# Optimization experiments

Measured on AMD Instinct MI355X. Metric: run time of the kernel, lower is better.

## Reference

```python
import jax, jax.numpy as jnp
import numpy as np

N, L, D, H = 4, 2048, 512, 8
DK = D // H


def setup_inputs() -> dict:
    key = jax.random.key(0)
    ks = jax.random.split(key, 12)
    s = 1.0 / np.sqrt(D)
    x_q = jax.random.normal(ks[0], (N, L, D), dtype=jnp.float32)
    x_k = jax.random.normal(ks[1], (N, L, D), dtype=jnp.float32)
    x_v = jax.random.normal(ks[2], (N, L, D), dtype=jnp.float32)
    # causal attention mask (1 = keep)
    attention_mask = jnp.tril(jnp.ones((L, L), dtype=jnp.int32))
    # padding mask: random valid lengths in [L//2, L], 1 = keep
    lengths = jax.random.randint(ks[3], (N,), L // 2, L + 1)
    padding_mask = (jnp.arange(L)[None, :] < lengths[:, None]).astype(jnp.int32)
    Wq = jax.random.uniform(ks[4], (D, D), jnp.float32, -s, s)
    bq = jax.random.uniform(ks[5], (D,), jnp.float32, -s, s)
    Wk = jax.random.uniform(ks[6], (D, D), jnp.float32, -s, s)
    bk = jax.random.uniform(ks[7], (D,), jnp.float32, -s, s)
    Wv = jax.random.uniform(ks[8], (D, D), jnp.float32, -s, s)
    bv = jax.random.uniform(ks[9], (D,), jnp.float32, -s, s)
    Wo = jax.random.uniform(ks[10], (D, D), jnp.float32, -s, s)
    bo = jax.random.uniform(ks[11], (D,), jnp.float32, -s, s)
    return {"x_q": x_q, "x_k": x_k, "x_v": x_v,
            "padding_mask": padding_mask, "attention_mask": attention_mask,
            "Wq": Wq, "bq": bq, "Wk": Wk, "bk": bk,
            "Wv": Wv, "bv": bv, "Wo": Wo, "bo": bo}


def reference(x_q, x_k, x_v, padding_mask, attention_mask,
              Wq, bq, Wk, bk, Wv, bv, Wo, bo):
    n, lq, _ = x_q.shape
    lkv = x_k.shape[1]
    Q = (x_q @ Wq.T + bq).reshape(n, lq, H, DK)
    K = (x_k @ Wk.T + bk).reshape(n, lkv, H, DK)
    V = (x_v @ Wv.T + bv).reshape(n, lkv, H, DK)
    # score: [n, lq, lkv, H]
    score = jnp.einsum('nihd,njhd->nijh', Q, K) / np.sqrt(DK)
    score = jnp.where(attention_mask.reshape(1, lq, lkv, 1) == 0, -jnp.inf, score)
    score = jnp.where(padding_mask.reshape(n, 1, lkv, 1) == 0, -jnp.inf, score)
    score = jax.nn.softmax(score, axis=2)
    value = jnp.einsum('nijh,njhd->nihd', score, V).reshape(n, lq, D)
    return value @ Wo.T + bo
```

## Files before the change

kernel.cpp:

```cpp
#include <hip/hip_runtime.h>
#include <hip/hip_bf16.h>

#define NB 4
#define LSEQ 2048
#define DMODEL 512
#define NH 8
#define DKH 64

typedef __attribute__((ext_vector_type(8))) short bf16x8;
typedef __attribute__((ext_vector_type(4))) float f32x4;

__device__ __forceinline__ unsigned short f2bf(float f) {
  __hip_bfloat16 h = __float2bfloat16(f);
  return __builtin_bit_cast(unsigned short, h);
}
__device__ __forceinline__ float bf2f(unsigned short u) {
  unsigned int x = ((unsigned int)u) << 16;
  return __builtin_bit_cast(float, x);
}

#define GLD16(gsrc, ldst)                                                     \
  __builtin_amdgcn_global_load_lds(                                           \
      (const __attribute__((address_space(1))) unsigned int*)(gsrc),          \
      (__attribute__((address_space(3))) unsigned int*)(ldst), 16, 0, 0)

__global__ __launch_bounds__(256) void prep(
    const float* __restrict__ s0, const float* __restrict__ s1,
    const float* __restrict__ s2, unsigned short* __restrict__ hi,
    unsigned short* __restrict__ lo,
    const float* __restrict__ w0, const float* __restrict__ w1,
    const float* __restrict__ w2, const float* __restrict__ w3,
    unsigned short* __restrict__ whi, unsigned short* __restrict__ wlo,
    int nz) {
  const int bid = blockIdx.x;
  const int actBlocks = nz << 12;
  const float* src;
  unsigned short *dh, *dl;
  int i;
  if (bid < actBlocks) {
    const int z = bid >> 12;
    src = (z == 0) ? s0 : (z == 1) ? s1 : s2;
    const size_t off = (size_t)z * ((size_t)NB * LSEQ * DMODEL);
    i = ((bid & 4095) * 256 + threadIdx.x) * 4;
    dh = hi + off; dl = lo + off;
  } else {
    const int wb = bid - actBlocks;
    const int wi = wb >> 8;
    src = (wi == 0) ? w0 : (wi == 1) ? w1 : (wi == 2) ? w2 : w3;
    const size_t off = (size_t)wi * 262144;
    i = ((wb & 255) * 256 + threadIdx.x) * 4;
    dh = whi + off; dl = wlo + off;
  }
  const float4 v = *(const float4*)&src[i];
  ushort4 h, l;
  h.x = f2bf(v.x); l.x = f2bf(v.x - bf2f(h.x));
  h.y = f2bf(v.y); l.y = f2bf(v.y - bf2f(h.y));
  h.z = f2bf(v.z); l.z = f2bf(v.z - bf2f(h.z));
  h.w = f2bf(v.w); l.w = f2bf(v.w - bf2f(h.w));
  *(ushort4*)&dh[i] = h;
  *(ushort4*)&dl[i] = l;
}

template <int BF16OUT>
__global__ __launch_bounds__(256, 1) void gemm3(
    const unsigned short* __restrict__ AhB, const unsigned short* __restrict__ AlB,
    const unsigned short* __restrict__ WhB, const unsigned short* __restrict__ WlB,
    const float* __restrict__ bias0, const float* __restrict__ bias1,
    const float* __restrict__ bias2, void* __restrict__ CB,
    unsigned short* __restrict__ VtOut, int zbase, int scaleq) {
  __shared__ unsigned short AsH[2][128 * 64];
  __shared__ unsigned short AsL[2][128 * 64];
  __shared__ unsigned short WsH[2][128 * 64];
  __shared__ unsigned short WsL[2][128 * 64];
  const size_t matE = (size_t)NB * LSEQ * DMODEL;

  const int bid = blockIdx.x;
  const int off = bid >> 3;
  const int P = (bid & 7) + 8 * (off >> 2);
  const int bx = off & 3;
  const int by = P & 63;
  const int z = P >> 6;
  const int zz = z + zbase;

  const unsigned short* Ah = AhB + (size_t)z * matE;
  const unsigned short* Al = AlB + (size_t)z * matE;
  const unsigned short* Wh = WhB + (size_t)z * DMODEL * DMODEL;
  const unsigned short* Wl = WlB + (size_t)z * DMODEL * DMODEL;
  const float* bias = (zz == 0) ? bias0 : (zz == 1) ? bias1 : bias2;
  const float scale = (scaleq && zz == 0) ? 0.18033688011112042f : 1.0f;
  const bool vt = BF16OUT && (zz == 2);

  const int tid = threadIdx.x;
  const int w = tid >> 6, lane = tid & 63;
  const int l15 = lane & 15, l4 = lane >> 4;
  const int bn = bx * 128;
  const int bm = by * 128;
  const int wm = (w >> 1) * 64, wn = (w & 1) * 64;
  const int lr8 = lane >> 3, slot = lane & 7;

  float bi[4];
#pragma unroll
  for (int nf = 0; nf < 4; ++nf) bi[nf] = bias[bn + wn + nf * 16 + l15];

  f32x4 acc[4][4] = {};

#define STAGE_G(buf, k0)                                                      \
  {                                                                           \
    _Pragma("unroll")                                                         \
    for (int j = 0; j < 4; ++j) {                                             \
      const int seg = w * 32 + j * 8;                                         \
      const int row = seg + lr8;                                              \
      const int sc = slot ^ (row & 7);                                        \
      const size_t gA = (size_t)(bm + row) * DMODEL + (k0) + sc * 8;          \
      const size_t gW = (size_t)(bn + row) * DMODEL + (k0) + sc * 8;          \
      GLD16(Ah + gA, &AsH[buf][seg * 64]);                                    \
      GLD16(Al + gA, &AsL[buf][seg * 64]);                                    \
      GLD16(Wh + gW, &WsH[buf][seg * 64]);                                    \
      GLD16(Wl + gW, &WsL[buf][seg * 64]);                                    \
    }                                                                         \
  }

  STAGE_G(0, 0);

#pragma unroll 1
  for (int it = 0; it < 8; ++it) {
    const int cur = it & 1;
    if (it < 7) {
      STAGE_G(cur ^ 1, (it + 1) * 64);
      asm volatile("s_waitcnt vmcnt(16)" ::: "memory");
    } else {
      asm volatile("s_waitcnt vmcnt(0)" ::: "memory");
    }
    __builtin_amdgcn_s_barrier();

#pragma unroll
    for (int ks = 0; ks < 2; ++ks) {
      bf16x8 afh[4], afl[4], wfh[4], wfl[4];
#pragma unroll
      for (int mf = 0; mf < 4; ++mf) {
        const int row = wm + mf * 16 + l15;
        const int sl = (ks * 4 + l4) ^ (row & 7);
        afh[mf] = *(const bf16x8*)&AsH[cur][row * 64 + sl * 8];
        afl[mf] = *(const bf16x8*)&AsL[cur][row * 64 + sl * 8];
      }
#pragma unroll
      for (int nf = 0; nf < 4; ++nf) {
        const int row = wn + nf * 16 + l15;
        const int sl = (ks * 4 + l4) ^ (row & 7);
        wfh[nf] = *(const bf16x8*)&WsH[cur][row * 64 + sl * 8];
        wfl[nf] = *(const bf16x8*)&WsL[cur][row * 64 + sl * 8];
      }
#pragma unroll
      for (int mf = 0; mf < 4; ++mf)
#pragma unroll
        for (int nf = 0; nf < 4; ++nf) {
          acc[mf][nf] = __builtin_amdgcn_mfma_f32_16x16x32_bf16(afh[mf], wfh[nf], acc[mf][nf], 0, 0, 0);
          acc[mf][nf] = __builtin_amdgcn_mfma_f32_16x16x32_bf16(afh[mf], wfl[nf], acc[mf][nf], 0, 0, 0);
          acc[mf][nf] = __builtin_amdgcn_mfma_f32_16x16x32_bf16(afl[mf], wfh[nf], acc[mf][nf], 0, 0, 0);
        }
    }
    __builtin_amdgcn_s_barrier();
  }
#undef STAGE_G

#pragma unroll
  for (int mf = 0; mf < 4; ++mf)
#pragma unroll
    for (int r = 0; r < 4; ++r) {
      const size_t row = (size_t)(bm + wm + mf * 16 + l4 * 4 + r);
#pragma unroll
      for (int nf = 0; nf < 4; ++nf) {
        const float v = (acc[mf][nf][r] + bi[nf]) * scale;
        const int col = bn + wn + nf * 16 + l15;
        if (vt) {
          const int tok = (int)row & (LSEQ - 1);
          const int nn = (int)row >> 11;
          const int hh = col >> 6, dd = col & 63;
          VtOut[((((size_t)nn * NH + hh) * DKH + dd) << 11) + tok] = f2bf(v);
        } else {
          const size_t o = row * DMODEL + col;
          if (BF16OUT) ((unsigned short*)CB)[z * matE + o] = f2bf(v);
          else         ((float*)CB)[z * matE + o] = v;
        }
      }
    }
}

__global__ __launch_bounds__(256, 3) void flash_mfma(
    const unsigned short* __restrict__ Qb, const unsigned short* __restrict__ Kb,
    const unsigned short* __restrict__ Vt, const int* __restrict__ pad,
    unsigned short* __restrict__ OH, unsigned short* __restrict__ OL) {
  __shared__ unsigned short Ks[2][64 * 64];
  __shared__ unsigned short Vs[2][64 * 64];
  __shared__ unsigned short Ps[64 * 64];
  __shared__ int s_nt;

  const int tid = threadIdx.x;
  const int bid = blockIdx.x;
  const int sub = bid >> 3;
  const int nh = (bid & 7) * 4 + (sub & 3);
  const int qt = 31 - (sub >> 2);
  const int n = nh >> 3, h = nh & 7;
  const int w = tid >> 6, lane = tid & 63;
  const int l15 = lane & 15, l4 = lane >> 4;
  const int lr8 = lane >> 3, slot = lane & 7;

  {
    const int v = (tid < 32) ? pad[(size_t)n * LSEQ + tid * 64] : 1;
    if (tid < 64) {
      const unsigned long long b = __ballot(v == 0);
      if (tid == 0) s_nt = b ? (int)(__ffsll(b) - 1) : 32;
    }
  }
  __syncthreads();
  const int nt = s_nt;

  int plast[4];
#pragma unroll
  for (int f = 0; f < 4; ++f)
    plast[f] = pad[(size_t)n * LSEQ + (nt - 1) * 64 + f * 16 + l15];

  bf16x8 vones;
  {
    const short o = (l15 == 0) ? (short)0x3F80 : (short)0;
#pragma unroll
    for (int j = 0; j < 8; ++j) vones[j] = o;
  }

  const size_t qrow = (size_t)(n * LSEQ + qt * 64 + w * 16 + l15) * DMODEL + h * DKH;
  const bf16x8 qa0 = *(const bf16x8*)(Qb + qrow + l4 * 8);
  const bf16x8 qa1 = *(const bf16x8*)(Qb + qrow + 32 + l4 * 8);

  f32x4 Oacc[5] = {};
  float m_[4];
#pragma unroll
  for (int r = 0; r < 4; ++r) m_[r] = -1e30f;

  const int ktend = (qt + 1 < nt) ? (qt + 1) : nt;

#pragma unroll
  for (int j = 0; j < 2; ++j) {
    const int seg = w * 16 + j * 8;
    const int row = seg + lr8;
    const int sc = slot ^ (row & 7);
    GLD16(Kb + (size_t)(n * LSEQ + row) * DMODEL + h * DKH + sc * 8, &Ks[0][seg * 64]);
    GLD16(Vt + ((size_t)nh * DKH + row) * LSEQ + sc * 8, &Vs[0][seg * 64]);
  }
  asm volatile("s_waitcnt vmcnt(0)" ::: "memory");
  __builtin_amdgcn_s_barrier();

#pragma unroll 1
  for (int kt = 0; kt < ktend; ++kt) {
    const int cur = kt & 1;
    if (kt + 1 < ktend) {
      const int nb = cur ^ 1;
#pragma unroll
      for (int j = 0; j < 2; ++j) {
        const int seg = w * 16 + j * 8;
        const int row = seg + lr8;
        const int sc = slot ^ (row & 7);
        GLD16(Kb + (size_t)(n * LSEQ + (kt + 1) * 64 + row) * DMODEL + h * DKH + sc * 8,
              &Ks[nb][seg * 64]);
        GLD16(Vt + ((size_t)nh * DKH + row) * LSEQ + (kt + 1) * 64 + sc * 8,
              &Vs[nb][seg * 64]);
      }
    }

    f32x4 S[4] = {};
#pragma unroll
    for (int f = 0; f < 4; ++f) {
      const int kr = f * 16 + l15;
      const int swz = kr & 7;
      const bf16x8 b0 = *(const bf16x8*)&Ks[cur][kr * 64 + ((l4 ^ swz) * 8)];
      S[f] = __builtin_amdgcn_mfma_f32_16x16x32_bf16(qa0, b0, S[f], 0, 0, 0);
      const bf16x8 b1 = *(const bf16x8*)&Ks[cur][kr * 64 + (((4 + l4) ^ swz) * 8)];
      S[f] = __builtin_amdgcn_mfma_f32_16x16x32_bf16(qa1, b1, S[f], 0, 0, 0);
    }

    if (kt == nt - 1) {
#pragma unroll
      for (int f = 0; f < 4; ++f)
        if (!plast[f]) {
#pragma unroll
          for (int r = 0; r < 4; ++r) S[f][r] = -1e30f;
        }
    }
    if (kt == qt) {
#pragma unroll
      for (int f = 0; f < 4; ++f) {
        const int col = f * 16 + l15;
#pragma unroll
        for (int r = 0; r < 4; ++r)
          if (col > w * 16 + l4 * 4 + r) S[f][r] = -1e30f;
      }
    }

    float pmax[4];
#pragma unroll
    for (int r = 0; r < 4; ++r)
      pmax[r] = fmaxf(fmaxf(S[0][r], S[1][r]), fmaxf(S[2][r], S[3][r]));
    const bool cond = (pmax[0] <= m_[0] + 11.f) && (pmax[1] <= m_[1] + 11.f) &&
                      (pmax[2] <= m_[2] + 11.f) && (pmax[3] <= m_[3] + 11.f);
    if (!__all(cond)) {
#pragma unroll
      for (int r = 0; r < 4; ++r) {
        float mx = pmax[r];
        mx = fmaxf(mx, __shfl_xor(mx, 1, 64));
        mx = fmaxf(mx, __shfl_xor(mx, 2, 64));
        mx = fmaxf(mx, __shfl_xor(mx, 4, 64));
        mx = fmaxf(mx, __shfl_xor(mx, 8, 64));
        const float mnew = fmaxf(m_[r], mx);
        const float alpha = exp2f(m_[r] - mnew);
        m_[r] = mnew;
#pragma unroll
        for (int f = 0; f < 5; ++f) Oacc[f][r] *= alpha;
      }
    }

#pragma unroll
    for (int r = 0; r < 4; ++r) {
      const int prow = w * 16 + l4 * 4 + r;
      const int psw = prow & 7;
#pragma unroll
      for (int f = 0; f < 4; ++f) {
        const float p = exp2f(S[f][r] - m_[r]);
        const int c16 = 2 * f + (l15 >> 3);
        Ps[prow * 64 + ((c16 ^ psw) * 8) + (lane & 7)] = f2bf(p);
      }
    }

#pragma unroll
    for (int ks = 0; ks < 2; ++ks) {
      const int prow = w * 16 + l15;
      const bf16x8 pa = *(const bf16x8*)&Ps[prow * 64 + (((ks * 4 + l4) ^ (prow & 7)) * 8)];
      Oacc[4] = __builtin_amdgcn_mfma_f32_16x16x32_bf16(pa, vones, Oacc[4], 0, 0, 0);
#pragma unroll
      for (int f = 0; f < 4; ++f) {
        const int vr = f * 16 + l15;
        const bf16x8 vb = *(const bf16x8*)&Vs[cur][vr * 64 + (((ks * 4 + l4) ^ (vr & 7)) * 8)];
        Oacc[f] = __builtin_amdgcn_mfma_f32_16x16x32_bf16(pa, vb, Oacc[f], 0, 0, 0);
      }
    }

    asm volatile("s_waitcnt vmcnt(0)" ::: "memory");
    __builtin_amdgcn_s_barrier();
  }

#pragma unroll
  for (int r = 0; r < 4; ++r) {
    const float lr = __shfl(Oacc[4][r], l4 << 4, 64);
    const float inv = 1.0f / lr;
    const size_t orow = (size_t)(n * LSEQ + qt * 64 + w * 16 + l4 * 4 + r) * DMODEL + h * DKH;
#pragma unroll
    for (int f = 0; f < 4; ++f) {
      const float v = Oacc[f][r] * inv;
      const unsigned short hh = f2bf(v);
      OH[orow + f * 16 + l15] = hh;
      OL[orow + f * 16 + l15] = f2bf(v - bf2f(hh));
    }
  }
}

extern "C" void kernel_launch(void* const* d_in, const int* in_sizes, int n_in,
                              void* d_out, int out_size, void* d_ws, size_t ws_size,
                              hipStream_t stream) {
  const float* x_q = (const float*)d_in[0];
  const float* x_k = (const float*)d_in[1];
  const float* x_v = (const float*)d_in[2];
  const int*   pad = (const int*)d_in[3];
  const float* Wq = (const float*)d_in[5];  const float* bq = (const float*)d_in[6];
  const float* Wk = (const float*)d_in[7];  const float* bk = (const float*)d_in[8];
  const float* Wv = (const float*)d_in[9];  const float* bv = (const float*)d_in[10];
  const float* Wo = (const float*)d_in[11]; const float* bo = (const float*)d_in[12];
  float* out = (float*)d_out;

  const size_t matE = (size_t)NB * LSEQ * DMODEL;
  const size_t wE = (size_t)DMODEL * DMODEL;
  unsigned short* base = (unsigned short*)d_ws;
  const size_t needB = (size_t)(9 * matE + 8 * wE) * 2;
  const bool batched = ws_size >= needB;

  if (batched) {
    unsigned short* Ah3 = base;
    unsigned short* Al3 = base + 3 * matE;
    unsigned short* QKV = base + 6 * matE;
    unsigned short* WhA = base + 9 * matE;
    unsigned short* WlA = WhA + 4 * wE;
    unsigned short* Vt  = QKV + 2 * matE;
    unsigned short* OHp = base;
    unsigned short* OLp = base + matE;

    prep<<<13312, 256, 0, stream>>>(x_q, x_k, x_v, Ah3, Al3,
                                    Wq, Wk, Wv, Wo, WhA, WlA, 3);
    gemm3<1><<<768, 256, 0, stream>>>(Ah3, Al3, WhA, WlA, bq, bk, bv,
                                      (void*)QKV, Vt, 0, 1);
    flash_mfma<<<1024, 256, 0, stream>>>(QKV, QKV + matE, Vt, pad, OHp, OLp);
    gemm3<0><<<256, 256, 0, stream>>>(OHp, OLp, WhA + 3 * wE, WlA + 3 * wE,
                                      bo, bo, bo, (void*)out, nullptr, 0, 0);
  } else {
    unsigned short* Ah = base;
    unsigned short* Al = base + matE;
    unsigned short* QKV = base + 2 * matE;
    unsigned short* WhA = base + 5 * matE;
    unsigned short* WlA = WhA + 4 * wE;
    unsigned short* Vt  = QKV + 2 * matE;
    unsigned short* OHp = base;
    unsigned short* OLp = base + matE;

    const float* xs[3] = {x_q, x_k, x_v};
    const float* bs[3] = {bq, bk, bv};
    for (int z = 0; z < 3; ++z) {
      prep<<<(z == 0) ? 5120 : 4096, 256, 0, stream>>>(
          xs[z], xs[z], xs[z], Ah, Al, Wq, Wk, Wv, Wo, WhA, WlA, 1);
      gemm3<1><<<256, 256, 0, stream>>>(Ah, Al, WhA + z * wE, WlA + z * wE,
                                        bs[z], bs[z], bs[z],
                                        (void*)(QKV + z * matE), Vt, z, 1);
    }
    flash_mfma<<<1024, 256, 0, stream>>>(QKV, QKV + matE, Vt, pad, OHp, OLp);
    gemm3<0><<<256, 256, 0, stream>>>(OHp, OLp, WhA + 3 * wE, WlA + 3 * wE,
                                      bo, bo, bo, (void*)out, nullptr, 0, 0);
  }
}
```

Before: 241.5 us.

## Replace bf16 hi/lo split GEMMs with single-pass fp16 across pipeline

Drops the three-MFMA bf16 hi/lo split emulation of fp32 in the projection GEMMs and writes one fp16 copy of activations and weights instead. Attention and all MFMAs switch from bf16 to fp16. This cuts MFMA work in the GEMMs to a third, halves the staging traffic and LDS use (which allows two blocks per CU), and removes the low-part writes from prep and flash. The cost is accuracy: inputs and the attention output lose precision, and fp16's narrower range could matter for unscaled values.

```diff
diff --git a/kernel.cpp b/kernel.cpp
--- a/kernel.cpp
+++ b/kernel.cpp
@@ -1,5 +1,4 @@
 #include <hip/hip_runtime.h>
-#include <hip/hip_bf16.h>
 
 #define NB 4
 #define LSEQ 2048
@@ -7,16 +6,12 @@
 #define NH 8
 #define DKH 64
 
-typedef __attribute__((ext_vector_type(8))) short bf16x8;
+typedef __attribute__((ext_vector_type(8))) _Float16 f16x8;
 typedef __attribute__((ext_vector_type(4))) float f32x4;
 
-__device__ __forceinline__ unsigned short f2bf(float f) {
-  __hip_bfloat16 h = __float2bfloat16(f);
+__device__ __forceinline__ unsigned short f2h(float f) {
+  _Float16 h = (_Float16)f;
   return __builtin_bit_cast(unsigned short, h);
-}
-__device__ __forceinline__ float bf2f(unsigned short u) {
-  unsigned int x = ((unsigned int)u) << 16;
-  return __builtin_bit_cast(float, x);
 }
 
 #define GLD16(gsrc, ldst)                                                     \
@@ -26,52 +21,41 @@
 
 __global__ __launch_bounds__(256) void prep(
     const float* __restrict__ s0, const float* __restrict__ s1,
-    const float* __restrict__ s2, unsigned short* __restrict__ hi,
-    unsigned short* __restrict__ lo,
+    const float* __restrict__ s2, unsigned short* __restrict__ xh,
     const float* __restrict__ w0, const float* __restrict__ w1,
     const float* __restrict__ w2, const float* __restrict__ w3,
-    unsigned short* __restrict__ whi, unsigned short* __restrict__ wlo,
-    int nz) {
+    unsigned short* __restrict__ wh, int nz) {
   const int bid = blockIdx.x;
   const int actBlocks = nz << 12;
   const float* src;
-  unsigned short *dh, *dl;
+  unsigned short* dst;
   int i;
   if (bid < actBlocks) {
     const int z = bid >> 12;
     src = (z == 0) ? s0 : (z == 1) ? s1 : s2;
-    const size_t off = (size_t)z * ((size_t)NB * LSEQ * DMODEL);
+    dst = xh + (size_t)z * ((size_t)NB * LSEQ * DMODEL);
     i = ((bid & 4095) * 256 + threadIdx.x) * 4;
-    dh = hi + off; dl = lo + off;
   } else {
     const int wb = bid - actBlocks;
     const int wi = wb >> 8;
     src = (wi == 0) ? w0 : (wi == 1) ? w1 : (wi == 2) ? w2 : w3;
-    const size_t off = (size_t)wi * 262144;
+    dst = wh + (size_t)wi * 262144;
     i = ((wb & 255) * 256 + threadIdx.x) * 4;
-    dh = whi + off; dl = wlo + off;
   }
   const float4 v = *(const float4*)&src[i];
-  ushort4 h, l;
-  h.x = f2bf(v.x); l.x = f2bf(v.x - bf2f(h.x));
-  h.y = f2bf(v.y); l.y = f2bf(v.y - bf2f(h.y));
-  h.z = f2bf(v.z); l.z = f2bf(v.z - bf2f(h.z));
-  h.w = f2bf(v.w); l.w = f2bf(v.w - bf2f(h.w));
-  *(ushort4*)&dh[i] = h;
-  *(ushort4*)&dl[i] = l;
-}
-
-template <int BF16OUT>
-__global__ __launch_bounds__(256, 1) void gemm3(
-    const unsigned short* __restrict__ AhB, const unsigned short* __restrict__ AlB,
-    const unsigned short* __restrict__ WhB, const unsigned short* __restrict__ WlB,
+  ushort4 o;
+  o.x = f2h(v.x); o.y = f2h(v.y); o.z = f2h(v.z); o.w = f2h(v.w);
+  *(ushort4*)&dst[i] = o;
+}
+
+template <int F16OUT>
+__global__ __launch_bounds__(256, 2) void gemm1(
+    const unsigned short* __restrict__ XhB, const unsigned short* __restrict__ WhB,
     const float* __restrict__ bias0, const float* __restrict__ bias1,
     const float* __restrict__ bias2, void* __restrict__ CB,
     unsigned short* __restrict__ VtOut, int zbase, int scaleq) {
-  __shared__ unsigned short AsH[2][128 * 64];
-  __shared__ unsigned short AsL[2][128 * 64];
-  __shared__ unsigned short WsH[2][128 * 64];
-  __shared__ unsigned short WsL[2][128 * 64];
+  __shared__ unsigned short As[2][128 * 64];
+  __shared__ unsigned short Ws[2][128 * 64];
   const size_t matE = (size_t)NB * LSEQ * DMODEL;
 
   const int bid = blockIdx.x;
@@ -82,13 +66,11 @@
   const int z = P >> 6;
   const int zz = z + zbase;
 
-  const unsigned short* Ah = AhB + (size_t)z * matE;
-  const unsigned short* Al = AlB + (size_t)z * matE;
+  const unsigned short* Xh = XhB + (size_t)z * matE;
   const unsigned short* Wh = WhB + (size_t)z * DMODEL * DMODEL;
-  const unsigned short* Wl = WlB + (size_t)z * DMODEL * DMODEL;
   const float* bias = (zz == 0) ? bias0 : (zz == 1) ? bias1 : bias2;
   const float scale = (scaleq && zz == 0) ? 0.18033688011112042f : 1.0f;
-  const bool vt = BF16OUT && (zz == 2);
+  const bool vt = F16OUT && (zz == 2);
 
   const int tid = threadIdx.x;
   const int w = tid >> 6, lane = tid & 63;
@@ -111,12 +93,10 @@
       const int seg = w * 32 + j * 8;                                         \
       const int row = seg + lr8;                                              \
       const int sc = slot ^ (row & 7);                                        \
-      const size_t gA = (size_t)(bm + row) * DMODEL + (k0) + sc * 8;          \
-      const size_t gW = (size_t)(bn + row) * DMODEL + (k0) + sc * 8;          \
-      GLD16(Ah + gA, &AsH[buf][seg * 64]);                                    \
-      GLD16(Al + gA, &AsL[buf][seg * 64]);                                    \
-      GLD16(Wh + gW, &WsH[buf][seg * 64]);                                    \
-      GLD16(Wl + gW, &WsL[buf][seg * 64]);                                    \
+      GLD16(Xh + (size_t)(bm + row) * DMODEL + (k0) + sc * 8,                 \
+            &As[buf][seg * 64]);                                              \
+      GLD16(Wh + (size_t)(bn + row) * DMODEL + (k0) + sc * 8,                 \
+            &Ws[buf][seg * 64]);                                              \
     }                                                                         \
   }
 
@@ -127,7 +107,7 @@
     const int cur = it & 1;
     if (it < 7) {
       STAGE_G(cur ^ 1, (it + 1) * 64);
-      asm volatile("s_waitcnt vmcnt(16)" ::: "memory");
+      asm volatile("s_waitcnt vmcnt(8)" ::: "memory");
     } else {
       asm volatile("s_waitcnt vmcnt(0)" ::: "memory");
     }
@@ -135,29 +115,24 @@
 
 #pragma unroll
     for (int ks = 0; ks < 2; ++ks) {
-      bf16x8 afh[4], afl[4], wfh[4], wfl[4];
+      f16x8 af[4], wf[4];
 #pragma unroll
       for (int mf = 0; mf < 4; ++mf) {
         const int row = wm + mf * 16 + l15;
         const int sl = (ks * 4 + l4) ^ (row & 7);
-        afh[mf] = *(const bf16x8*)&AsH[cur][row * 64 + sl * 8];
-        afl[mf] = *(const bf16x8*)&AsL[cur][row * 64 + sl * 8];
+        af[mf] = *(const f16x8*)&As[cur][row * 64 + sl * 8];
       }
 #pragma unroll
       for (int nf = 0; nf < 4; ++nf) {
         const int row = wn + nf * 16 + l15;
         const int sl = (ks * 4 + l4) ^ (row & 7);
-        wfh[nf] = *(const bf16x8*)&WsH[cur][row * 64 + sl * 8];
-        wfl[nf] = *(const bf16x8*)&WsL[cur][row * 64 + sl * 8];
+        wf[nf] = *(const f16x8*)&Ws[cur][row * 64 + sl * 8];
       }
 #pragma unroll
       for (int mf = 0; mf < 4; ++mf)
 #pragma unroll
-        for (int nf = 0; nf < 4; ++nf) {
-          acc[mf][nf] = __builtin_amdgcn_mfma_f32_16x16x32_bf16(afh[mf], wfh[nf], acc[mf][nf], 0, 0, 0);
-          acc[mf][nf] = __builtin_amdgcn_mfma_f32_16x16x32_bf16(afh[mf], wfl[nf], acc[mf][nf], 0, 0, 0);
-          acc[mf][nf] = __builtin_amdgcn_mfma_f32_16x16x32_bf16(afl[mf], wfh[nf], acc[mf][nf], 0, 0, 0);
-        }
+        for (int nf = 0; nf < 4; ++nf)
+          acc[mf][nf] = __builtin_amdgcn_mfma_f32_16x16x32_f16(af[mf], wf[nf], acc[mf][nf], 0, 0, 0);
     }
     __builtin_amdgcn_s_barrier();
   }
@@ -176,11 +151,11 @@
           const int tok = (int)row & (LSEQ - 1);
           const int nn = (int)row >> 11;
           const int hh = col >> 6, dd = col & 63;
-          VtOut[((((size_t)nn * NH + hh) * DKH + dd) << 11) + tok] = f2bf(v);
+          VtOut[((((size_t)nn * NH + hh) * DKH + dd) << 11) + tok] = f2h(v);
         } else {
           const size_t o = row * DMODEL + col;
-          if (BF16OUT) ((unsigned short*)CB)[z * matE + o] = f2bf(v);
-          else         ((float*)CB)[z * matE + o] = v;
+          if (F16OUT) ((unsigned short*)CB)[z * matE + o] = f2h(v);
+          else        ((float*)CB)[z * matE + o] = v;
         }
       }
     }
@@ -189,7 +164,7 @@
 __global__ __launch_bounds__(256, 3) void flash_mfma(
     const unsigned short* __restrict__ Qb, const unsigned short* __restrict__ Kb,
     const unsigned short* __restrict__ Vt, const int* __restrict__ pad,
-    unsigned short* __restrict__ OH, unsigned short* __restrict__ OL) {
+    unsigned short* __restrict__ OH) {
   __shared__ unsigned short Ks[2][64 * 64];
   __shared__ unsigned short Vs[2][64 * 64];
   __shared__ unsigned short Ps[64 * 64];
@@ -220,16 +195,13 @@
   for (int f = 0; f < 4; ++f)
     plast[f] = pad[(size_t)n * LSEQ + (nt - 1) * 64 + f * 16 + l15];
 
-  bf16x8 vones;
-  {
-    const short o = (l15 == 0) ? (short)0x3F80 : (short)0;
-#pragma unroll
-    for (int j = 0; j < 8; ++j) vones[j] = o;
-  }
+  f16x8 vones;
+#pragma unroll
+  for (int j = 0; j < 8; ++j) vones[j] = (_Float16)((l15 == 0) ? 1.0f : 0.0f);
 
   const size_t qrow = (size_t)(n * LSEQ + qt * 64 + w * 16 + l15) * DMODEL + h * DKH;
-  const bf16x8 qa0 = *(const bf16x8*)(Qb + qrow + l4 * 8);
-  const bf16x8 qa1 = *(const bf16x8*)(Qb + qrow + 32 + l4 * 8);
+  const f16x8 qa0 = *(const f16x8*)(Qb + qrow + l4 * 8);
+  const f16x8 qa1 = *(const f16x8*)(Qb + qrow + 32 + l4 * 8);
 
   f32x4 Oacc[5] = {};
   float m_[4];
@@ -271,10 +243,10 @@
     for (int f = 0; f < 4; ++f) {
       const int kr = f * 16 + l15;
       const int swz = kr & 7;
-      const bf16x8 b0 = *(const bf16x8*)&Ks[cur][kr * 64 + ((l4 ^ swz) * 8)];
-      S[f] = __builtin_amdgcn_mfma_f32_16x16x32_bf16(qa0, b0, S[f], 0, 0, 0);
-      const bf16x8 b1 = *(const bf16x8*)&Ks[cur][kr * 64 + (((4 + l4) ^ swz) * 8)];
-      S[f] = __builtin_amdgcn_mfma_f32_16x16x32_bf16(qa1, b1, S[f], 0, 0, 0);
+      const f16x8 b0 = *(const f16x8*)&Ks[cur][kr * 64 + ((l4 ^ swz) * 8)];
+      S[f] = __builtin_amdgcn_mfma_f32_16x16x32_f16(qa0, b0, S[f], 0, 0, 0);
+      const f16x8 b1 = *(const f16x8*)&Ks[cur][kr * 64 + (((4 + l4) ^ swz) * 8)];
+      S[f] = __builtin_amdgcn_mfma_f32_16x16x32_f16(qa1, b1, S[f], 0, 0, 0);
     }
 
     if (kt == nt - 1) {
@@ -325,20 +297,20 @@
       for (int f = 0; f < 4; ++f) {
         const float p = exp2f(S[f][r] - m_[r]);
         const int c16 = 2 * f + (l15 >> 3);
-        Ps[prow * 64 + ((c16 ^ psw) * 8) + (lane & 7)] = f2bf(p);
+        Ps[prow * 64 + ((c16 ^ psw) * 8) + (lane & 7)] = f2h(p);
       }
     }
 
 #pragma unroll
     for (int ks = 0; ks < 2; ++ks) {
       const int prow = w * 16 + l15;
-      const bf16x8 pa = *(const bf16x8*)&Ps[prow * 64 + (((ks * 4 + l4) ^ (prow & 7)) * 8)];
-      Oacc[4] = __builtin_amdgcn_mfma_f32_16x16x32_bf16(pa, vones, Oacc[4], 0, 0, 0);
+      const f16x8 pa = *(const f16x8*)&Ps[prow * 64 + (((ks * 4 + l4) ^ (prow & 7)) * 8)];
+      Oacc[4] = __builtin_amdgcn_mfma_f32_16x16x32_f16(pa, vones, Oacc[4], 0, 0, 0);
 #pragma unroll
       for (int f = 0; f < 4; ++f) {
         const int vr = f * 16 + l15;
-        const bf16x8 vb = *(const bf16x8*)&Vs[cur][vr * 64 + (((ks * 4 + l4) ^ (vr & 7)) * 8)];
-        Oacc[f] = __builtin_amdgcn_mfma_f32_16x16x32_bf16(pa, vb, Oacc[f], 0, 0, 0);
+        const f16x8 vb = *(const f16x8*)&Vs[cur][vr * 64 + (((ks * 4 + l4) ^ (vr & 7)) * 8)];
+        Oacc[f] = __builtin_amdgcn_mfma_f32_16x16x32_f16(pa, vb, Oacc[f], 0, 0, 0);
       }
     }
 
@@ -352,12 +324,8 @@
     const float inv = 1.0f / lr;
     const size_t orow = (size_t)(n * LSEQ + qt * 64 + w * 16 + l4 * 4 + r) * DMODEL + h * DKH;
 #pragma unroll
-    for (int f = 0; f < 4; ++f) {
-      const float v = Oacc[f][r] * inv;
-      const unsigned short hh = f2bf(v);
-      OH[orow + f * 16 + l15] = hh;
-      OL[orow + f * 16 + l15] = f2bf(v - bf2f(hh));
-    }
+    for (int f = 0; f < 4; ++f)
+      OH[orow + f * 16 + l15] = f2h(Oacc[f][r] * inv);
   }
 }
 
@@ -377,47 +345,38 @@
   const size_t matE = (size_t)NB * LSEQ * DMODEL;
   const size_t wE = (size_t)DMODEL * DMODEL;
   unsigned short* base = (unsigned short*)d_ws;
-  const size_t needB = (size_t)(9 * matE + 8 * wE) * 2;
+  const size_t needB = (size_t)(6 * matE + 4 * wE) * 2;
   const bool batched = ws_size >= needB;
 
   if (batched) {
-    unsigned short* Ah3 = base;
-    unsigned short* Al3 = base + 3 * matE;
-    unsigned short* QKV = base + 6 * matE;
-    unsigned short* WhA = base + 9 * matE;
-    unsigned short* WlA = WhA + 4 * wE;
+    unsigned short* Xh  = base;
+    unsigned short* Wh4 = base + 3 * matE;
+    unsigned short* QKV = Wh4 + 4 * wE;
     unsigned short* Vt  = QKV + 2 * matE;
-    unsigned short* OHp = base;
-    unsigned short* OLp = base + matE;
-
-    prep<<<13312, 256, 0, stream>>>(x_q, x_k, x_v, Ah3, Al3,
-                                    Wq, Wk, Wv, Wo, WhA, WlA, 3);
-    gemm3<1><<<768, 256, 0, stream>>>(Ah3, Al3, WhA, WlA, bq, bk, bv,
-                                      (void*)QKV, Vt, 0, 1);
-    flash_mfma<<<1024, 256, 0, stream>>>(QKV, QKV + matE, Vt, pad, OHp, OLp);
-    gemm3<0><<<256, 256, 0, stream>>>(OHp, OLp, WhA + 3 * wE, WlA + 3 * wE,
-                                      bo, bo, bo, (void*)out, nullptr, 0, 0);
+    unsigned short* OH  = base;
+
+    prep<<<13312, 256, 0, stream>>>(x_q, x_k, x_v, Xh, Wq, Wk, Wv, Wo, Wh4, 3);
+    gemm1<1><<<768, 256, 0, stream>>>(Xh, Wh4, bq, bk, bv, (void*)QKV, Vt, 0, 1);
+    flash_mfma<<<1024, 256, 0, stream>>>(QKV, QKV + matE, Vt, pad, OH);
+    gemm1<0><<<256, 256, 0, stream>>>(OH, Wh4 + 3 * wE, bo, bo, bo,
+                                      (void*)out, nullptr, 0, 0);
   } else {
-    unsigned short* Ah = base;
-    unsigned short* Al = base + matE;
-    unsigned short* QKV = base + 2 * matE;
-    unsigned short* WhA = base + 5 * matE;
-    unsigned short* WlA = WhA + 4 * wE;
+    unsigned short* Xh  = base;
+    unsigned short* Wh4 = base + matE;
+    unsigned short* QKV = Wh4 + 4 * wE;
     unsigned short* Vt  = QKV + 2 * matE;
-    unsigned short* OHp = base;
-    unsigned short* OLp = base + matE;
+    unsigned short* OH  = base;
 
     const float* xs[3] = {x_q, x_k, x_v};
     const float* bs[3] = {bq, bk, bv};
     for (int z = 0; z < 3; ++z) {
       prep<<<(z == 0) ? 5120 : 4096, 256, 0, stream>>>(
-          xs[z], xs[z], xs[z], Ah, Al, Wq, Wk, Wv, Wo, WhA, WlA, 1);
-      gemm3<1><<<256, 256, 0, stream>>>(Ah, Al, WhA + z * wE, WlA + z * wE,
-                                        bs[z], bs[z], bs[z],
+          xs[z], xs[z], xs[z], Xh, Wq, Wk, Wv, Wo, Wh4, 1);
+      gemm1<1><<<256, 256, 0, stream>>>(Xh, Wh4 + z * wE, bs[z], bs[z], bs[z],
                                         (void*)(QKV + z * matE), Vt, z, 1);
     }
-    flash_mfma<<<1024, 256, 0, stream>>>(QKV, QKV + matE, Vt, pad, OHp, OLp);
-    gemm3<0><<<256, 256, 0, stream>>>(OHp, OLp, WhA + 3 * wE, WlA + 3 * wE,
-                                      bo, bo, bo, (void*)out, nullptr, 0, 0);
-  }
-}
+    flash_mfma<<<1024, 256, 0, stream>>>(QKV, QKV + matE, Vt, pad, OH);
+    gemm1<0><<<256, 256, 0, stream>>>(OH, Wh4 + 3 * wE, bo, bo, bo,
+                                      (void*)out, nullptr, 0, 0);
+  }
+}
```

Result: faster. 200.7 us (-16.9%).
